# Optimization experiments

Hardware: AMD Instinct MI355X
Metric: run time of the kernel (lower is better)

Reference implementation:

```python
import jax, jax.numpy as jnp
import numpy as np

GAMA = 10.0


def setup_inputs() -> dict:
    key = jax.random.key(0)
    k1, k2, k3, k4, k5 = jax.random.split(key, 5)
    n_class, n_center, hidden, batch = 100, 4, 512, 512
    init_mu, sigma_lower = 0.1, 10.0
    x = jax.random.normal(k1, (batch, hidden), dtype=jnp.float32)
    y = jax.random.randint(k2, (batch,), 0, n_class, dtype=jnp.int32).astype(jnp.int64)
    mu_base_vector = jax.random.normal(k3, (hidden,), dtype=jnp.float32)
    class_mu = jax.random.uniform(k4, (n_class, n_center, hidden), dtype=jnp.float32) * (2 * init_mu) - init_mu
    class_sigma = jnp.ones((n_class, n_center, hidden), dtype=jnp.float32) * sigma_lower
    class_pi = jax.random.uniform(k5, (n_class, n_center), dtype=jnp.float32)
    class_pi = class_pi / class_pi.sum(axis=1, keepdims=True)
    return {"x": x, "y": y, "mu_base_vector": mu_base_vector,
            "class_mu": class_mu, "class_sigma": class_sigma, "class_pi": class_pi}


def reference(x, y, mu_base_vector, class_mu, class_sigma, class_pi):
    # Cluster.log_likelihood(x, y, reduction='mean')
    B, H = x.shape
    # scale() detaches mu_base_vector
    xs = (x - jax.lax.stop_gradient(mu_base_vector)) / GAMA  # [B, H]
    # log_probs: broadcasted diagonal-Gaussian log-likelihood
    diff = xs[None, None, :, :] - class_mu[:, :, None, :]            # [C, K, B, H]
    log_exp = -0.5 * jnp.sum(diff * diff * (class_sigma * class_sigma)[:, :, None, :], axis=-1)  # [C, K, B]
    log_det = jnp.sum(jnp.log(class_sigma), axis=-1)[:, :, None]     # [C, K, 1]
    const = -0.5 * H * jnp.log(2.0 * jnp.pi).astype(x.dtype)
    log_probs = jnp.transpose(log_exp + log_det + const, (2, 0, 1))  # [B, C, K]
    # one-hot class selection == gather along class axis
    lp_sel = jnp.take_along_axis(log_probs, y[:, None, None].astype(jnp.int32), axis=1)[:, 0, :]  # [B, K]
    log_pi = jnp.log(jax.nn.softmax(class_pi, axis=1))[y]            # [B, K]
    log_scores = log_pi + lp_sel                                     # [B, K]
    log_likelihood = jnp.max(log_scores, axis=1)                     # [B]
    return jnp.mean(log_likelihood)
```

## Files before the change

### kernel.cpp

```cpp
#include <hip/hip_runtime.h>
#include <math.h>

#define KCENTERS 4
#define GAMA_INV 0.1f

__global__ void __launch_bounds__(256)
cluster_ll_kernel(const float* __restrict__ x,
                  const int* __restrict__ y,
                  const float* __restrict__ mu_base,
                  const float* __restrict__ class_mu,
                  const float* __restrict__ class_sigma,
                  const float* __restrict__ class_pi,
                  float* __restrict__ out,
                  int B, int H) {
    const int i    = blockIdx.x;
    const int tid  = threadIdx.x;
    const int wave = tid >> 6;
    const int lane = tid & 63;

    const int c = y[i];

    const float* __restrict__ xi = x + (size_t)i * H;
    const float* __restrict__ mu = class_mu    + ((size_t)c * KCENTERS + wave) * H;
    const float* __restrict__ sg = class_sigma + ((size_t)c * KCENTERS + wave) * H;

    float acc  = 0.0f;
    float ldet = 0.0f;
    for (int h = lane; h < H; h += 64) {
        float xs = (xi[h] - mu_base[h]) * GAMA_INV;
        float d  = xs - mu[h];
        float s  = sg[h];
        acc  = fmaf(d * d, s * s, acc);
        ldet += logf(s);
    }
    #pragma unroll
    for (int off = 32; off > 0; off >>= 1) {
        acc  += __shfl_down(acc,  off, 64);
        ldet += __shfl_down(ldet, off, 64);
    }

    __shared__ float scores[KCENTERS];
    if (lane == 0) {
        float p[KCENTERS];
        float m = -INFINITY;
        #pragma unroll
        for (int k = 0; k < KCENTERS; ++k) {
            p[k] = class_pi[(size_t)c * KCENTERS + k];
            m = fmaxf(m, p[k]);
        }
        float se = 0.0f;
        #pragma unroll
        for (int k = 0; k < KCENTERS; ++k) se += expf(p[k] - m);
        float lse = m + logf(se);

        const float cst = -0.5f * (float)H * logf(2.0f * (float)M_PI);
        scores[wave] = (p[wave] - lse) + (-0.5f * acc + ldet + cst);
    }
    __syncthreads();

    if (tid == 0) {
        float mx = scores[0];
        #pragma unroll
        for (int k = 1; k < KCENTERS; ++k) mx = fmaxf(mx, scores[k]);
        atomicAdd(out, mx / (float)B);
    }
}

extern "C" void kernel_launch(void* const* d_in, const int* in_sizes, int n_in,
                              void* d_out, int out_size, void* d_ws, size_t ws_size,
                              hipStream_t stream) {
    const float* x        = (const float*)d_in[0];
    const int*   y        = (const int*)  d_in[1];
    const float* mu_base  = (const float*)d_in[2];
    const float* class_mu = (const float*)d_in[3];
    const float* class_sg = (const float*)d_in[4];
    const float* class_pi = (const float*)d_in[5];
    float* out = (float*)d_out;

    const int B = in_sizes[1];
    const int H = in_sizes[2];

    hipMemsetAsync(out, 0, sizeof(float), stream);

    cluster_ll_kernel<<<B, 256, 0, stream>>>(x, y, mu_base, class_mu, class_sg,
                                             class_pi, out, B, H);
}
```

Measured before the change: 75.65 us.

## Use one wave per row with float4 loads and two-pass mean reduction

Each row is now handled by a single 64-lane wave that loops over the four centers, reusing the scaled x values held in registers and loading with float4. The atomicAdd plus memset is replaced by a per-row workspace write followed by a small mean kernel, and fast __logf/__expf intrinsics replace the libm calls. The loop is hardcoded to NITER=2, so it assumes H=512, and it adds a second kernel launch.

```diff
diff --git a/kernel.cpp b/kernel.cpp
--- a/kernel.cpp
+++ b/kernel.cpp
@@ -1,69 +1,94 @@
 #include <hip/hip_runtime.h>
 #include <math.h>
 
-#define KCENTERS 4
+#define KC 4
 #define GAMA_INV 0.1f
+#define NITER 2
 
-__global__ void __launch_bounds__(256)
-cluster_ll_kernel(const float* __restrict__ x,
-                  const int* __restrict__ y,
-                  const float* __restrict__ mu_base,
-                  const float* __restrict__ class_mu,
-                  const float* __restrict__ class_sigma,
-                  const float* __restrict__ class_pi,
-                  float* __restrict__ out,
-                  int B, int H) {
+__global__ void __launch_bounds__(64)
+row_ll_kernel(const float* __restrict__ x,
+              const int* __restrict__ y,
+              const float* __restrict__ mu_base,
+              const float* __restrict__ class_mu,
+              const float* __restrict__ class_sigma,
+              const float* __restrict__ class_pi,
+              float* __restrict__ rowll, int H) {
     const int i    = blockIdx.x;
-    const int tid  = threadIdx.x;
-    const int wave = tid >> 6;
-    const int lane = tid & 63;
+    const int lane = threadIdx.x;
+    const int c    = y[i];
 
-    const int c = y[i];
+    const float4* __restrict__ x4  = (const float4*)(x + (size_t)i * H);
+    const float4* __restrict__ mb4 = (const float4*)mu_base;
 
-    const float* __restrict__ xi = x + (size_t)i * H;
-    const float* __restrict__ mu = class_mu    + ((size_t)c * KCENTERS + wave) * H;
-    const float* __restrict__ sg = class_sigma + ((size_t)c * KCENTERS + wave) * H;
-
-    float acc  = 0.0f;
-    float ldet = 0.0f;
-    for (int h = lane; h < H; h += 64) {
-        float xs = (xi[h] - mu_base[h]) * GAMA_INV;
-        float d  = xs - mu[h];
-        float s  = sg[h];
-        acc  = fmaf(d * d, s * s, acc);
-        ldet += logf(s);
-    }
+    float4 xs[NITER];
     #pragma unroll
-    for (int off = 32; off > 0; off >>= 1) {
-        acc  += __shfl_down(acc,  off, 64);
-        ldet += __shfl_down(ldet, off, 64);
+    for (int j = 0; j < NITER; ++j) {
+        float4 a = x4[lane + 64 * j];
+        float4 b = mb4[lane + 64 * j];
+        xs[j].x = (a.x - b.x) * GAMA_INV;
+        xs[j].y = (a.y - b.y) * GAMA_INV;
+        xs[j].z = (a.z - b.z) * GAMA_INV;
+        xs[j].w = (a.w - b.w) * GAMA_INV;
     }
 
-    __shared__ float scores[KCENTERS];
+    float sc[KC];
+    #pragma unroll
+    for (int k = 0; k < KC; ++k) {
+        const float4* __restrict__ mu4 =
+            (const float4*)(class_mu + ((size_t)c * KC + k) * H);
+        const float4* __restrict__ sg4 =
+            (const float4*)(class_sigma + ((size_t)c * KC + k) * H);
+        float acc = 0.0f, ldet = 0.0f;
+        #pragma unroll
+        for (int j = 0; j < NITER; ++j) {
+            float4 m = mu4[lane + 64 * j];
+            float4 s = sg4[lane + 64 * j];
+            float dx = xs[j].x - m.x, dy = xs[j].y - m.y;
+            float dz = xs[j].z - m.z, dw = xs[j].w - m.w;
+            acc = fmaf(dx * dx, s.x * s.x, acc);
+            acc = fmaf(dy * dy, s.y * s.y, acc);
+            acc = fmaf(dz * dz, s.z * s.z, acc);
+            acc = fmaf(dw * dw, s.w * s.w, acc);
+            ldet += __logf(s.x) + __logf(s.y) + __logf(s.z) + __logf(s.w);
+        }
+        #pragma unroll
+        for (int off = 1; off < 64; off <<= 1) {
+            acc  += __shfl_xor(acc,  off, 64);
+            ldet += __shfl_xor(ldet, off, 64);
+        }
+        sc[k] = -0.5f * acc + ldet;
+    }
+
     if (lane == 0) {
-        float p[KCENTERS];
+        float p[KC];
         float m = -INFINITY;
         #pragma unroll
-        for (int k = 0; k < KCENTERS; ++k) {
-            p[k] = class_pi[(size_t)c * KCENTERS + k];
+        for (int k = 0; k < KC; ++k) {
+            p[k] = class_pi[(size_t)c * KC + k];
             m = fmaxf(m, p[k]);
         }
         float se = 0.0f;
         #pragma unroll
-        for (int k = 0; k < KCENTERS; ++k) se += expf(p[k] - m);
-        float lse = m + logf(se);
+        for (int k = 0; k < KC; ++k) se += __expf(p[k] - m);
+        float lse = m + __logf(se);
 
-        const float cst = -0.5f * (float)H * logf(2.0f * (float)M_PI);
-        scores[wave] = (p[wave] - lse) + (-0.5f * acc + ldet + cst);
+        const float cst = -0.5f * (float)H * __logf(2.0f * (float)M_PI);
+        float mx = -INFINITY;
+        #pragma unroll
+        for (int k = 0; k < KC; ++k)
+            mx = fmaxf(mx, (p[k] - lse) + sc[k] + cst);
+        rowll[i] = mx;
     }
-    __syncthreads();
+}
 
-    if (tid == 0) {
-        float mx = scores[0];
-        #pragma unroll
-        for (int k = 1; k < KCENTERS; ++k) mx = fmaxf(mx, scores[k]);
-        atomicAdd(out, mx / (float)B);
-    }
+__global__ void __launch_bounds__(64)
+mean_kernel(const float* __restrict__ rowll, float* __restrict__ out, int B) {
+    const int lane = threadIdx.x;
+    float s = 0.0f;
+    for (int j = lane; j < B; j += 64) s += rowll[j];
+    #pragma unroll
+    for (int off = 1; off < 64; off <<= 1) s += __shfl_xor(s, off, 64);
+    if (lane == 0) out[0] = s / (float)B;
 }
 
 extern "C" void kernel_launch(void* const* d_in, const int* in_sizes, int n_in,
@@ -75,13 +100,13 @@
     const float* class_mu = (const float*)d_in[3];
     const float* class_sg = (const float*)d_in[4];
     const float* class_pi = (const float*)d_in[5];
-    float* out = (float*)d_out;
+    float* out   = (float*)d_out;
+    float* rowll = (float*)d_ws;
 
     const int B = in_sizes[1];
     const int H = in_sizes[2];
 
-    hipMemsetAsync(out, 0, sizeof(float), stream);
-
-    cluster_ll_kernel<<<B, 256, 0, stream>>>(x, y, mu_base, class_mu, class_sg,
-                                             class_pi, out, B, H);
+    row_ll_kernel<<<B, 64, 0, stream>>>(x, y, mu_base, class_mu, class_sg,
+                                        class_pi, rowll, H);
+    mean_kernel<<<1, 64, 0, stream>>>(rowll, out, B);
 }
```

After: 68.79 us. -9.1%, faster.
